# Performance work log

Measured on AMD Instinct MI355X. Metric: run time of the kernel, lower is better.

## Reference

```python
import jax, jax.numpy as jnp
import numpy as np
import math

B, S, H = 2, 2048, 2048
NH, NKV, HD = 16, 4, 128


def _rope_tables(seq_len, head_dim):
    # Standard RoPE: freqs over half dim, duplicated to full head_dim.
    inv_freq = 1.0 / (10000.0 ** (np.arange(0, head_dim, 2, dtype=np.float32) / head_dim))
    t = np.arange(seq_len, dtype=np.float32)
    freqs = np.outer(t, inv_freq)  # [S, HD/2]
    emb = np.concatenate([freqs, freqs], axis=-1)  # [S, HD]
    return jnp.asarray(np.cos(emb)), jnp.asarray(np.sin(emb))


def setup_inputs() -> dict:
    key = jax.random.key(0)
    k1, k2, k3, k4 = jax.random.split(key, 4)
    cos, sin = _rope_tables(S, HD)
    return {
        "x": jax.random.normal(k1, (B, S, H), dtype=jnp.float32),
        "cos": cos,
        "sin": sin,
        "Wq": jax.random.normal(k2, (H, NH * HD), dtype=jnp.float32) * (1.0 / math.sqrt(H)),
        "Wkv": jax.random.normal(k3, (H, 2 * NKV * HD), dtype=jnp.float32) * (1.0 / math.sqrt(H)),
        "Wo": jax.random.normal(k4, (NH * HD, H), dtype=jnp.float32) * (1.0 / math.sqrt(NH * HD)),
    }


def _rotate_half(x):
    x1, x2 = jnp.split(x, 2, axis=-1)
    return jnp.concatenate([-x2, x1], axis=-1)


def _apply_rotary(x, cos, sin):
    # x: [B, S, nheads, HD]; cos/sin: [S, HD]
    c = cos[None, :, None, :]
    s = sin[None, :, None, :]
    return x * c + _rotate_half(x) * s


def reference(x, cos, sin, Wq, Wkv, Wo):
    b, s, _ = x.shape
    q = (x @ Wq).reshape(b, s, NH, HD)
    kv = x @ Wkv
    k, v = jnp.split(kv, [NKV * HD], axis=-1)
    k = k.reshape(b, s, NKV, HD)
    v = v.reshape(b, s, NKV, HD)
    q = _apply_rotary(q, cos, sin)
    k = _apply_rotary(k, cos, sin)
    # to [B, heads, S, HD]
    q = jnp.transpose(q, (0, 2, 1, 3))
    k = jnp.transpose(k, (0, 2, 1, 3))
    v = jnp.transpose(v, (0, 2, 1, 3))
    # GQA: repeat K/V heads
    rep = NH // NKV
    k = jnp.repeat(k, rep, axis=1)
    v = jnp.repeat(v, rep, axis=1)
    scale = jnp.asarray(1.0 / math.sqrt(HD), dtype=x.dtype)
    scores = jnp.einsum('bhqd,bhkd->bhqk', q * scale, k)  # [B, NH, S, S]
    causal = jnp.tril(jnp.ones((s, s), dtype=jnp.bool_))
    scores = jnp.where(causal, scores, jnp.asarray(-jnp.inf, scores.dtype))
    attn = jax.nn.softmax(scores, axis=-1)
    out = jnp.einsum('bhqk,bhkd->bhqd', attn, v)
    out = jnp.transpose(out, (0, 2, 1, 3)).reshape(b, s, NH * HD)
    return out @ Wo
```

## Files before the change

### kernel.cpp

```cpp
#include <hip/hip_runtime.h>
#include <math.h>

#define NB 2
#define SEQ 2048
#define HDIM 2048
#define NHD 16
#define NKVH 4
#define HEADD 128
#define MROWS (NB*SEQ)
#define NQCOLS (NHD*HEADD)
#define QKVCOLS 3072

typedef unsigned short ushortT;
typedef __attribute__((ext_vector_type(8))) short short8;
typedef __attribute__((ext_vector_type(4))) float floatx4;
typedef __attribute__((ext_vector_type(4))) unsigned short ushort4v;

__device__ __forceinline__ ushortT f2bf(float f) {
  union { float f; unsigned int u; } v; v.f = f;
  unsigned int r = v.u + 0x7FFFu + ((v.u >> 16) & 1u);
  return (ushortT)(r >> 16);
}
__device__ __forceinline__ float bf2f(ushortT u) {
  union { unsigned int u; float f; } v; v.u = ((unsigned int)u) << 16;
  return v.f;
}

__device__ __forceinline__ unsigned int cvt_pk_bf16(float lo, float hi) {
  unsigned int r;
  asm("v_cvt_pk_bf16_f32 %0, %1, %2" : "=v"(r) : "v"(lo), "v"(hi));
  return r;
}

__device__ __forceinline__ void gload16(const ushortT* g, ushortT* l) {
  __builtin_amdgcn_global_load_lds(
      (const __attribute__((address_space(1))) void*)g,
      (__attribute__((address_space(3))) void*)l, 16, 0, 0);
}

__device__ __forceinline__ void tile_barrier() {
  asm volatile("" ::: "memory");
  __builtin_amdgcn_s_barrier();
  asm volatile("" ::: "memory");
  __builtin_amdgcn_sched_barrier(0);
}

__global__ __launch_bounds__(256) void cast_bf16_kernel(
    const float* __restrict__ in, ushortT* __restrict__ out, int n4) {
  int i = blockIdx.x * 256 + threadIdx.x;
  if (i >= n4) return;
  float4 v = ((const float4*)in)[i];
  ushort4v o;
  o.x = f2bf(v.x); o.y = f2bf(v.y); o.z = f2bf(v.z); o.w = f2bf(v.w);
  ((ushort4v*)out)[i] = o;
}

__global__ __launch_bounds__(256) void transpose_cast3_kernel(
    const float* __restrict__ Wq, const float* __restrict__ Wkv,
    const float* __restrict__ Wo, ushortT* __restrict__ out) {
  __shared__ ushortT tile[32][33];
  int cu0 = blockIdx.x * 32, r0 = blockIdx.y * 32;
  const float* src; int C, c0;
  if (cu0 < 2048)      { src = Wq;  C = 2048; c0 = cu0; }
  else if (cu0 < 3072) { src = Wkv; C = 1024; c0 = cu0 - 2048; }
  else                 { src = Wo;  C = 2048; c0 = cu0 - 3072; }
  int tx = threadIdx.x & 31, ty = threadIdx.x >> 5;
#pragma unroll
  for (int i = 0; i < 4; ++i)
    tile[ty + i*8][tx] = f2bf(src[(size_t)(r0 + ty + i*8) * C + c0 + tx]);
  __syncthreads();
#pragma unroll
  for (int i = 0; i < 4; ++i)
    out[(size_t)(cu0 + ty + i*8) * 2048 + r0 + tx] = tile[tx][ty + i*8];
}

template <int MH>
__global__ __launch_bounds__(512, 2) void gemm_ring_kernel(
    const ushortT* __restrict__ A, const ushortT* __restrict__ Bt,
    void* __restrict__ C, int M, int N, int K, int c_fp32) {
  constexpr int BM = 128 * MH;
  constexpr int LPT = MH + 2;
  __shared__ __align__(16) ushortT lA[4][BM * 32];
  __shared__ __align__(16) ushortT lB[4][256 * 32];
  const int m0 = blockIdx.y * BM;
  const int n0 = blockIdx.x * 256;
  const int tid = threadIdx.x;
  const int lane = tid & 63, wave = tid >> 6;
  const int g = lane >> 4, l15 = lane & 15;
  const int wr = wave >> 2, wc = wave & 3;
  const int wm = wr * (BM / 2), wn = wc * 64;

  floatx4 acc[4 * MH][4] = {};

  auto stageA = [&](int u) {
    ushortT* dst = lA[u & 3];
    const int kt = u << 5;
#pragma unroll
    for (int i = 0; i < MH; ++i) {
      int s = i * 512 + tid;
      int r = s >> 2, j = s & 3;
      int jj = j ^ ((r >> 1) & 3);
      gload16(A + (size_t)(m0 + r) * K + kt + jj * 8, dst + s * 8);
    }
  };
  auto stageB = [&](int u) {
    ushortT* dst = lB[u & 3];
    const int kt = u << 5;
#pragma unroll
    for (int i = 0; i < 2; ++i) {
      int s = i * 512 + tid;
      int r = s >> 2, j = s & 3;
      int jj = j ^ ((r >> 1) & 3);
      gload16(Bt + (size_t)(n0 + r) * K + kt + jj * 8, dst + s * 8);
    }
  };

  stageA(0); stageB(0); stageA(1); stageB(1); stageA(2); stageB(2);

  const int NT = K >> 5;
  for (int u = 0; u < NT; ++u) {
    if constexpr (MH == 2) {
      if (u + 2 < NT)      asm volatile("s_waitcnt vmcnt(8)" ::: "memory");
      else if (u + 1 < NT) asm volatile("s_waitcnt vmcnt(4)" ::: "memory");
      else                 asm volatile("s_waitcnt vmcnt(0)" ::: "memory");
    } else {
      if (u + 2 < NT)      asm volatile("s_waitcnt vmcnt(6)" ::: "memory");
      else if (u + 1 < NT) asm volatile("s_waitcnt vmcnt(3)" ::: "memory");
      else                 asm volatile("s_waitcnt vmcnt(0)" ::: "memory");
    }
    tile_barrier();

    const ushortT* la = lA[u & 3];
    const ushortT* lb = lB[u & 3];
    const bool more = (u + 3) < NT;

    short8 bfr[4];
#pragma unroll
    for (int nt = 0; nt < 4; ++nt) {
      int col = wn + nt * 16 + l15;
      bfr[nt] = *(const short8*)(lb + col * 32 + (g ^ ((col >> 1) & 3)) * 8);
    }

#pragma unroll
    for (int mh = 0; mh < MH; ++mh) {
      if (mh) tile_barrier();
      short8 afr[4];
#pragma unroll
      for (int mt = 0; mt < 4; ++mt) {
        int row = wm + mh * 64 + mt * 16 + l15;
        afr[mt] = *(const short8*)(la + row * 32 + (g ^ ((row >> 1) & 3)) * 8);
      }
      if (more) {
        if (mh == 0) stageA(u + 3);
        if (mh == MH - 1) stageB(u + 3);
      }
      __builtin_amdgcn_s_setprio(1);
#pragma unroll
      for (int mt = 0; mt < 4; ++mt)
#pragma unroll
        for (int nt = 0; nt < 4; ++nt)
          acc[mh * 4 + mt][nt] = __builtin_amdgcn_mfma_f32_16x16x32_bf16(
              afr[mt], bfr[nt], acc[mh * 4 + mt][nt], 0, 0, 0);
      __builtin_amdgcn_s_setprio(0);
    }
  }

#pragma unroll
  for (int fm = 0; fm < 4 * MH; ++fm)
#pragma unroll
    for (int nt = 0; nt < 4; ++nt)
#pragma unroll
      for (int r4 = 0; r4 < 4; ++r4) {
        int row = m0 + wm + fm * 16 + g * 4 + r4;
        int col = n0 + wn + nt * 16 + l15;
        float v = acc[fm][nt][r4];
        if (c_fp32) ((float*)C)[(size_t)row * N + col] = v;
        else ((ushortT*)C)[(size_t)row * N + col] = f2bf(v);
      }
}

__global__ __launch_bounds__(256) void rope_qk_kernel(
    const ushortT* __restrict__ QKVtmp, const float* __restrict__ cosT,
    const float* __restrict__ sinT, ushortT* __restrict__ Qr,
    ushortT* __restrict__ Kr) {
  int idx = blockIdx.x * 256 + threadIdx.x;
  if (idx < NB * SEQ * NHD * 64) {
    int d = idx & 63;
    int t = idx >> 6;
    int h = t & (NHD - 1);
    int bs = t >> 4;
    int s = bs & (SEQ - 1);
    int b = bs >> 11;
    float c = cosT[s * HEADD + d], sn = sinT[s * HEADD + d];
    float q1 = bf2f(QKVtmp[(size_t)bs * QKVCOLS + h * HEADD + d]);
    float q2 = bf2f(QKVtmp[(size_t)bs * QKVCOLS + h * HEADD + d + 64]);
    size_t o = ((size_t)(b * NHD + h) * SEQ + s) * HEADD + d;
    Qr[o]      = f2bf(q1 * c - q2 * sn);
    Qr[o + 64] = f2bf(q2 * c + q1 * sn);
  } else {
    int k = idx - NB * SEQ * NHD * 64;
    int d = k & 63;
    int t = k >> 6;
    int kvh = t & (NKVH - 1);
    int bs = t >> 2;
    int s = bs & (SEQ - 1);
    int b = bs >> 11;
    float c = cosT[s * HEADD + d], sn = sinT[s * HEADD + d];
    float k1 = bf2f(QKVtmp[(size_t)bs * QKVCOLS + 2048 + kvh * HEADD + d]);
    float k2 = bf2f(QKVtmp[(size_t)bs * QKVCOLS + 2048 + kvh * HEADD + d + 64]);
    size_t o = ((size_t)(b * NKVH + kvh) * SEQ + s) * HEADD + d;
    Kr[o]      = f2bf(k1 * c - k2 * sn);
    Kr[o + 64] = f2bf(k2 * c + k1 * sn);
  }
}

__global__ __launch_bounds__(256) void v_relayout_kernel(
    const ushortT* __restrict__ QKVtmp, ushortT* __restrict__ Vt) {
  __shared__ ushortT tile[32][33];
  int bk = blockIdx.z;
  int b = bk >> 2, kvh = bk & 3;
  int s0 = blockIdx.x * 32, d0 = blockIdx.y * 32;
  int tx = threadIdx.x & 31, ty = threadIdx.x >> 5;
#pragma unroll
  for (int i = 0; i < 4; ++i) {
    int s = s0 + ty + i * 8;
    tile[ty + i * 8][tx] =
        QKVtmp[(size_t)(b * SEQ + s) * QKVCOLS + 2560 + kvh * HEADD + d0 + tx];
  }
  __syncthreads();
#pragma unroll
  for (int i = 0; i < 4; ++i) {
    int d = d0 + ty + i * 8;
    Vt[((size_t)bk * HEADD + d) * SEQ + s0 + tx] = tile[tx][ty + i * 8];
  }
}

__global__ __launch_bounds__(256) void attn_kernel(
    const ushortT* __restrict__ Q,
    const ushortT* __restrict__ Kg,
    const ushortT* __restrict__ Vg,
    ushortT* __restrict__ Oa) {
  __shared__ __align__(16) ushortT lK[2][64 * 128];
  __shared__ __align__(16) ushortT lV[2][128 * 64];
  __shared__ __align__(16) ushortT lP[4 * 16 * 64];

  const int tid = threadIdx.x;
  const int w = tid >> 6, lane = tid & 63;
  const int g = lane >> 4, l15 = lane & 15;
  const int sw = l15 & 7;
  const int bh = blockIdx.x;
  const int b = bh >> 4, h = bh & 15;
  const int kvh = h >> 2;
  const int yi = blockIdx.y;
  const int qiA = 31 - yi;
  const int qiB = yi;
  const int nA = qiA + 1, nB = qiB + 1;

  const float SC = 0.08838834764831845f * 1.4426950408889634f;
  const float THR = 8.0f / SC;

  const ushortT* kbase = Kg + ((size_t)(b * NKVH + kvh)) * SEQ * HEADD;
  const ushortT* vbase = Vg + ((size_t)(b * NKVH + kvh)) * HEADD * SEQ;
  ushortT* pw = lP + w * 16 * 64;

  const int qwA = (qiA << 6) + w * 16;
  const int qwB = (qiB << 6) + w * 16;

  short8 qfA[4], qfB[4];
  {
    const ushortT* qpA = Q + (((size_t)(b * NHD + h)) * SEQ + qwA + l15) * HEADD + g * 8;
    const ushortT* qpB = Q + (((size_t)(b * NHD + h)) * SEQ + qwB + l15) * HEADD + g * 8;
#pragma unroll
    for (int ks = 0; ks < 4; ++ks) {
      qfA[ks] = *(const short8*)(qpA + ks * 32);
      qfB[ks] = *(const short8*)(qpB + ks * 32);
    }
  }

  floatx4 o[8] = {};
  float m_s = -INFINITY;
  float l_s = 0.f;

  auto stage = [&](int kt, int buf) {
#pragma unroll
    for (int ii = 0; ii < 4; ++ii) {
      int s = ii * 256 + tid;
      int r = s >> 4, j = (s & 15) ^ (r & 7);
      gload16(kbase + (size_t)(kt * 64 + r) * HEADD + j * 8, lK[buf] + s * 8);
    }
#pragma unroll
    for (int ii = 0; ii < 4; ++ii) {
      int s = ii * 256 + tid;
      int r = s >> 3, j = (s & 7) ^ (r & 7);
      gload16(vbase + (size_t)r * SEQ + kt * 64 + j * 8, lV[buf] + s * 8);
    }
  };

  auto compute = [&](const short8 (&qf)[4], int qw, int kt, int cur) {
    const int rel = qw - kt * 64;

    floatx4 sc4[4] = {};
    __builtin_amdgcn_s_setprio(1);
#pragma unroll
    for (int nt = 0; nt < 4; ++nt) {
      if (nt * 16 > rel + 15) continue;
#pragma unroll
      for (int ks = 0; ks < 4; ++ks) {
        short8 kf = *(const short8*)(lK[cur] + (nt * 16 + l15) * 128 + ((ks * 4 + g) ^ sw) * 8);
        sc4[nt] = __builtin_amdgcn_mfma_f32_16x16x32_bf16(kf, qf[ks], sc4[nt], 0, 0, 0);
      }
    }
    __builtin_amdgcn_s_setprio(0);

    const bool needmask = (kt * 64 + 63) > qw;
    float ps[4][4];
    float mx = -INFINITY;
#pragma unroll
    for (int nt = 0; nt < 4; ++nt)
#pragma unroll
      for (int r = 0; r < 4; ++r) {
        float v = sc4[nt][r];
        if (needmask) {
          int kg = kt * 64 + nt * 16 + g * 4 + r;
          if (kg > qw + l15) v = -INFINITY;
        }
        ps[nt][r] = v;
        mx = fmaxf(mx, v);
      }
    mx = fmaxf(mx, __shfl_xor(mx, 16));
    mx = fmaxf(mx, __shfl_xor(mx, 32));

    float mn;
    if (__all(mx <= m_s + THR)) {
      mn = m_s;
    } else {
      mn = fmaxf(m_s, mx);
      float alpha = __builtin_amdgcn_exp2f((m_s - mn) * SC);
      l_s *= alpha;
#pragma unroll
      for (int dt = 0; dt < 8; ++dt)
#pragma unroll
        for (int r = 0; r < 4; ++r) o[dt][r] *= alpha;
      m_s = mn;
    }
    const float mnSC = mn * SC;

    float rs = 0.f;
#pragma unroll
    for (int nt = 0; nt < 4; ++nt) {
      float e[4];
#pragma unroll
      for (int r = 0; r < 4; ++r) {
        e[r] = __builtin_amdgcn_exp2f(__builtin_fmaf(ps[nt][r], SC, -mnSC));
        rs += e[r];
      }
      uint2 pk;
      pk.x = cvt_pk_bf16(e[0], e[1]);
      pk.y = cvt_pk_bf16(e[2], e[3]);
      *(uint2*)(pw + l15 * 64 + (((nt * 2 + (g >> 1)) ^ sw) * 8 + (g & 1) * 4)) = pk;
    }
    rs += __shfl_xor(rs, 16);
    rs += __shfl_xor(rs, 32);
    l_s += rs;

    __builtin_amdgcn_s_setprio(1);
#pragma unroll
    for (int ks = 0; ks < 2; ++ks) {
      if (kt * 64 + ks * 32 > qw + 15) continue;
      short8 bp = *(const short8*)(pw + l15 * 64 + ((ks * 4 + g) ^ sw) * 8);
#pragma unroll
      for (int dt = 0; dt < 8; ++dt) {
        short8 vf = *(const short8*)(lV[cur] + (dt * 16 + l15) * 64 + ((ks * 4 + g) ^ sw) * 8);
        o[dt] = __builtin_amdgcn_mfma_f32_16x16x32_bf16(vf, bp, o[dt], 0, 0, 0);
      }
    }
    __builtin_amdgcn_s_setprio(0);
  };

  auto epilogue = [&](int qw) {
    float inv = 1.f / l_s;
    int qg = qw + l15;
#pragma unroll
    for (int dt = 0; dt < 8; ++dt) {
      uint2 ov;
      ov.x = cvt_pk_bf16(o[dt][0] * inv, o[dt][1] * inv);
      ov.y = cvt_pk_bf16(o[dt][2] * inv, o[dt][3] * inv);
      *(uint2*)(Oa + (size_t)(b * SEQ + qg) * NQCOLS + h * HEADD + dt * 16 + g * 4) = ov;
    }
  };

  stage(0, 0);
  asm volatile("s_waitcnt vmcnt(0)" ::: "memory");
  __builtin_amdgcn_s_barrier();

  for (int kt = 0; kt < nA; ++kt) {
    const int cur = kt & 1;
    if (kt + 1 < nA) stage(kt + 1, cur ^ 1);
    else             stage(0, cur ^ 1);
    compute(qfA, qwA, kt, cur);
    asm volatile("s_waitcnt vmcnt(0)" ::: "memory");
    __builtin_amdgcn_s_barrier();
  }
  epilogue(qwA);
#pragma unroll
  for (int dt = 0; dt < 8; ++dt) o[dt] = floatx4{0.f, 0.f, 0.f, 0.f};
  m_s = -INFINITY; l_s = 0.f;

  for (int kt = 0; kt < nB; ++kt) {
    const int cur = (nA + kt) & 1;
    if (kt + 1 < nB) stage(kt + 1, cur ^ 1);
    compute(qfB, qwB, kt, cur);
    asm volatile("s_waitcnt vmcnt(0)" ::: "memory");
    __builtin_amdgcn_s_barrier();
  }
  epilogue(qwB);
}

extern "C" void kernel_launch(void* const* d_in, const int* in_sizes, int n_in,
                              void* d_out, int out_size, void* d_ws, size_t ws_size,
                              hipStream_t stream) {
  const float* x    = (const float*)d_in[0];
  const float* cosT = (const float*)d_in[1];
  const float* sinT = (const float*)d_in[2];
  const float* Wq   = (const float*)d_in[3];
  const float* Wkv  = (const float*)d_in[4];
  const float* Wo   = (const float*)d_in[5];

  char* ws = (char*)d_ws;
  ushortT* x_bf   = (ushortT*)(ws + 0);
  ushortT* Wqkvt  = (ushortT*)(ws + 16777216);
  ushortT* Wot    = (ushortT*)(ws + 29360128);
  ushortT* QKVtmp = (ushortT*)(ws + 37748736);
  ushortT* Qr     = (ushortT*)(ws + 62914560);
  ushortT* Kr     = (ushortT*)(ws + 79691776);
  ushortT* Vt     = (ushortT*)(ws + 83886080);
  ushortT* Oattn  = QKVtmp;

  cast_bf16_kernel<<<8192, 256, 0, stream>>>(x, x_bf, (MROWS * HDIM) / 4);
  transpose_cast3_kernel<<<dim3(160, 64), 256, 0, stream>>>(Wq, Wkv, Wo, Wqkvt);

  gemm_ring_kernel<2><<<dim3(12, 16), 512, 0, stream>>>(x_bf, Wqkvt, QKVtmp,
                                                        MROWS, QKVCOLS, HDIM, 0);

  rope_qk_kernel<<<20480, 256, 0, stream>>>(QKVtmp, cosT, sinT, Qr, Kr);
  v_relayout_kernel<<<dim3(64, 4, 8), 256, 0, stream>>>(QKVtmp, Vt);

  attn_kernel<<<dim3(32, 16), 256, 0, stream>>>(Qr, Kr, Vt, Oattn);

  gemm_ring_kernel<1><<<dim3(8, 32), 512, 0, stream>>>(Oattn, Wot, d_out,
                                                       MROWS, HDIM, NQCOLS, 1);
}
```

Measured before the change: 313.6 us.

## Enlarge attention query tile to 128 rows with two m-tiles per wave

Each attention block now handles one 128-row query tile, with every wave owning 32 rows as two 16-row MFMA m-tiles. Each K and V fragment read from LDS feeds two MFMAs, cutting LDS traffic and staging per query, and loads are amortised over more work. This replaces the earlier pairing of a short and a long causal tile per block, so block work is now uneven; heavy tiles are ordered first to soften the tail. Register pressure roughly doubles for accumulators, and launch bounds now request two blocks per CU.

```diff
diff --git a/kernel.cpp b/kernel.cpp
--- a/kernel.cpp
+++ b/kernel.cpp
@@ -79,7 +79,6 @@
     const ushortT* __restrict__ A, const ushortT* __restrict__ Bt,
     void* __restrict__ C, int M, int N, int K, int c_fp32) {
   constexpr int BM = 128 * MH;
-  constexpr int LPT = MH + 2;
   __shared__ __align__(16) ushortT lA[4][BM * 32];
   __shared__ __align__(16) ushortT lB[4][256 * 32];
   const int m0 = blockIdx.y * BM;
@@ -235,14 +234,14 @@
   }
 }
 
-__global__ __launch_bounds__(256) void attn_kernel(
+__global__ __launch_bounds__(256, 2) void attn_kernel(
     const ushortT* __restrict__ Q,
     const ushortT* __restrict__ Kg,
     const ushortT* __restrict__ Vg,
     ushortT* __restrict__ Oa) {
   __shared__ __align__(16) ushortT lK[2][64 * 128];
   __shared__ __align__(16) ushortT lV[2][128 * 64];
-  __shared__ __align__(16) ushortT lP[4 * 16 * 64];
+  __shared__ __align__(16) ushortT lP[4 * 32 * 64];
 
   const int tid = threadIdx.x;
   const int w = tid >> 6, lane = tid & 63;
@@ -252,34 +251,30 @@
   const int b = bh >> 4, h = bh & 15;
   const int kvh = h >> 2;
   const int yi = blockIdx.y;
-  const int qiA = 31 - yi;
-  const int qiB = yi;
-  const int nA = qiA + 1, nB = qiB + 1;
+  const int qi = (yi < 8) ? (15 - yi) : (yi - 8);
+  const int q0 = qi << 7;
+  const int qw = q0 + w * 32;
+  const int nkt = 2 * qi + 2;
 
   const float SC = 0.08838834764831845f * 1.4426950408889634f;
   const float THR = 8.0f / SC;
 
   const ushortT* kbase = Kg + ((size_t)(b * NKVH + kvh)) * SEQ * HEADD;
   const ushortT* vbase = Vg + ((size_t)(b * NKVH + kvh)) * HEADD * SEQ;
-  ushortT* pw = lP + w * 16 * 64;
-
-  const int qwA = (qiA << 6) + w * 16;
-  const int qwB = (qiB << 6) + w * 16;
-
-  short8 qfA[4], qfB[4];
-  {
-    const ushortT* qpA = Q + (((size_t)(b * NHD + h)) * SEQ + qwA + l15) * HEADD + g * 8;
-    const ushortT* qpB = Q + (((size_t)(b * NHD + h)) * SEQ + qwB + l15) * HEADD + g * 8;
-#pragma unroll
-    for (int ks = 0; ks < 4; ++ks) {
-      qfA[ks] = *(const short8*)(qpA + ks * 32);
-      qfB[ks] = *(const short8*)(qpB + ks * 32);
-    }
-  }
-
-  floatx4 o[8] = {};
-  float m_s = -INFINITY;
-  float l_s = 0.f;
+  ushortT* pw = lP + w * 32 * 64;
+
+  short8 qf[2][4];
+#pragma unroll
+  for (int mt = 0; mt < 2; ++mt) {
+    const ushortT* qp =
+        Q + (((size_t)(b * NHD + h)) * SEQ + qw + mt * 16 + l15) * HEADD + g * 8;
+#pragma unroll
+    for (int ks = 0; ks < 4; ++ks) qf[mt][ks] = *(const short8*)(qp + ks * 32);
+  }
+
+  floatx4 o[2][8] = {};
+  float m_s[2] = {-INFINITY, -INFINITY};
+  float l_s[2] = {0.f, 0.f};
 
   auto stage = [&](int kt, int buf) {
 #pragma unroll
@@ -296,124 +291,126 @@
     }
   };
 
-  auto compute = [&](const short8 (&qf)[4], int qw, int kt, int cur) {
-    const int rel = qw - kt * 64;
-
-    floatx4 sc4[4] = {};
-    __builtin_amdgcn_s_setprio(1);
-#pragma unroll
-    for (int nt = 0; nt < 4; ++nt) {
-      if (nt * 16 > rel + 15) continue;
-#pragma unroll
-      for (int ks = 0; ks < 4; ++ks) {
-        short8 kf = *(const short8*)(lK[cur] + (nt * 16 + l15) * 128 + ((ks * 4 + g) ^ sw) * 8);
-        sc4[nt] = __builtin_amdgcn_mfma_f32_16x16x32_bf16(kf, qf[ks], sc4[nt], 0, 0, 0);
-      }
-    }
-    __builtin_amdgcn_s_setprio(0);
-
-    const bool needmask = (kt * 64 + 63) > qw;
-    float ps[4][4];
-    float mx = -INFINITY;
-#pragma unroll
-    for (int nt = 0; nt < 4; ++nt)
-#pragma unroll
-      for (int r = 0; r < 4; ++r) {
-        float v = sc4[nt][r];
-        if (needmask) {
-          int kg = kt * 64 + nt * 16 + g * 4 + r;
-          if (kg > qw + l15) v = -INFINITY;
-        }
-        ps[nt][r] = v;
-        mx = fmaxf(mx, v);
-      }
-    mx = fmaxf(mx, __shfl_xor(mx, 16));
-    mx = fmaxf(mx, __shfl_xor(mx, 32));
-
-    float mn;
-    if (__all(mx <= m_s + THR)) {
-      mn = m_s;
-    } else {
-      mn = fmaxf(m_s, mx);
-      float alpha = __builtin_amdgcn_exp2f((m_s - mn) * SC);
-      l_s *= alpha;
-#pragma unroll
-      for (int dt = 0; dt < 8; ++dt)
-#pragma unroll
-        for (int r = 0; r < 4; ++r) o[dt][r] *= alpha;
-      m_s = mn;
-    }
-    const float mnSC = mn * SC;
-
-    float rs = 0.f;
-#pragma unroll
-    for (int nt = 0; nt < 4; ++nt) {
-      float e[4];
-#pragma unroll
-      for (int r = 0; r < 4; ++r) {
-        e[r] = __builtin_amdgcn_exp2f(__builtin_fmaf(ps[nt][r], SC, -mnSC));
-        rs += e[r];
-      }
-      uint2 pk;
-      pk.x = cvt_pk_bf16(e[0], e[1]);
-      pk.y = cvt_pk_bf16(e[2], e[3]);
-      *(uint2*)(pw + l15 * 64 + (((nt * 2 + (g >> 1)) ^ sw) * 8 + (g & 1) * 4)) = pk;
-    }
-    rs += __shfl_xor(rs, 16);
-    rs += __shfl_xor(rs, 32);
-    l_s += rs;
-
-    __builtin_amdgcn_s_setprio(1);
-#pragma unroll
-    for (int ks = 0; ks < 2; ++ks) {
-      if (kt * 64 + ks * 32 > qw + 15) continue;
-      short8 bp = *(const short8*)(pw + l15 * 64 + ((ks * 4 + g) ^ sw) * 8);
-#pragma unroll
-      for (int dt = 0; dt < 8; ++dt) {
-        short8 vf = *(const short8*)(lV[cur] + (dt * 16 + l15) * 64 + ((ks * 4 + g) ^ sw) * 8);
-        o[dt] = __builtin_amdgcn_mfma_f32_16x16x32_bf16(vf, bp, o[dt], 0, 0, 0);
-      }
-    }
-    __builtin_amdgcn_s_setprio(0);
-  };
-
-  auto epilogue = [&](int qw) {
-    float inv = 1.f / l_s;
-    int qg = qw + l15;
-#pragma unroll
-    for (int dt = 0; dt < 8; ++dt) {
-      uint2 ov;
-      ov.x = cvt_pk_bf16(o[dt][0] * inv, o[dt][1] * inv);
-      ov.y = cvt_pk_bf16(o[dt][2] * inv, o[dt][3] * inv);
-      *(uint2*)(Oa + (size_t)(b * SEQ + qg) * NQCOLS + h * HEADD + dt * 16 + g * 4) = ov;
-    }
-  };
-
   stage(0, 0);
   asm volatile("s_waitcnt vmcnt(0)" ::: "memory");
   __builtin_amdgcn_s_barrier();
 
-  for (int kt = 0; kt < nA; ++kt) {
+  for (int kt = 0; kt < nkt; ++kt) {
     const int cur = kt & 1;
-    if (kt + 1 < nA) stage(kt + 1, cur ^ 1);
-    else             stage(0, cur ^ 1);
-    compute(qfA, qwA, kt, cur);
+    if (kt + 1 < nkt) stage(kt + 1, cur ^ 1);
+
+    const int kb = kt * 64;
+    const int rel0 = qw - kb;
+    const int rel1 = qw + 16 - kb;
+
+    floatx4 sc[2][4] = {};
+    __builtin_amdgcn_s_setprio(1);
+#pragma unroll
+    for (int nt = 0; nt < 4; ++nt) {
+      if (nt * 16 > rel1 + 15) continue;
+      const bool need0 = (nt * 16 <= rel0 + 15);
+#pragma unroll
+      for (int ks = 0; ks < 4; ++ks) {
+        short8 kf = *(const short8*)(lK[cur] + (nt * 16 + l15) * 128 + ((ks * 4 + g) ^ sw) * 8);
+        sc[1][nt] = __builtin_amdgcn_mfma_f32_16x16x32_bf16(kf, qf[1][ks], sc[1][nt], 0, 0, 0);
+        if (need0)
+          sc[0][nt] = __builtin_amdgcn_mfma_f32_16x16x32_bf16(kf, qf[0][ks], sc[0][nt], 0, 0, 0);
+      }
+    }
+    __builtin_amdgcn_s_setprio(0);
+
+#pragma unroll
+    for (int mt = 0; mt < 2; ++mt) {
+      const int qsub = qw + mt * 16;
+      if (kb > qsub + 15) continue;
+      const bool needmask = (kb + 63) > qsub;
+      float ps[4][4];
+      float mx = -INFINITY;
+#pragma unroll
+      for (int nt = 0; nt < 4; ++nt)
+#pragma unroll
+        for (int r = 0; r < 4; ++r) {
+          float v = sc[mt][nt][r];
+          if (needmask) {
+            int kg = kb + nt * 16 + g * 4 + r;
+            if (kg > qsub + l15) v = -INFINITY;
+          }
+          ps[nt][r] = v;
+          mx = fmaxf(mx, v);
+        }
+      mx = fmaxf(mx, __shfl_xor(mx, 16));
+      mx = fmaxf(mx, __shfl_xor(mx, 32));
+
+      float mn;
+      if (__all(mx <= m_s[mt] + THR)) {
+        mn = m_s[mt];
+      } else {
+        mn = fmaxf(m_s[mt], mx);
+        float alpha = __builtin_amdgcn_exp2f((m_s[mt] - mn) * SC);
+        l_s[mt] *= alpha;
+#pragma unroll
+        for (int dt = 0; dt < 8; ++dt)
+#pragma unroll
+          for (int r = 0; r < 4; ++r) o[mt][dt][r] *= alpha;
+        m_s[mt] = mn;
+      }
+      const float mnSC = mn * SC;
+
+      float rs = 0.f;
+#pragma unroll
+      for (int nt = 0; nt < 4; ++nt) {
+        float e[4];
+#pragma unroll
+        for (int r = 0; r < 4; ++r) {
+          e[r] = __builtin_amdgcn_exp2f(__builtin_fmaf(ps[nt][r], SC, -mnSC));
+          rs += e[r];
+        }
+        uint2 pk;
+        pk.x = cvt_pk_bf16(e[0], e[1]);
+        pk.y = cvt_pk_bf16(e[2], e[3]);
+        *(uint2*)(pw + (mt * 16 + l15) * 64 +
+                  (((nt * 2 + (g >> 1)) ^ sw) * 8 + (g & 1) * 4)) = pk;
+      }
+      rs += __shfl_xor(rs, 16);
+      rs += __shfl_xor(rs, 32);
+      l_s[mt] += rs;
+    }
+
+    __builtin_amdgcn_s_setprio(1);
+#pragma unroll
+    for (int ks = 0; ks < 2; ++ks) {
+      const bool n1 = (kb + ks * 32 <= qw + 31);
+      if (!n1) continue;
+      const bool n0 = (kb + ks * 32 <= qw + 15);
+      short8 bp1 = *(const short8*)(pw + (16 + l15) * 64 + ((ks * 4 + g) ^ sw) * 8);
+      short8 bp0;
+      if (n0) bp0 = *(const short8*)(pw + l15 * 64 + ((ks * 4 + g) ^ sw) * 8);
+#pragma unroll
+      for (int dt = 0; dt < 8; ++dt) {
+        short8 vf = *(const short8*)(lV[cur] + (dt * 16 + l15) * 64 + ((ks * 4 + g) ^ sw) * 8);
+        o[1][dt] = __builtin_amdgcn_mfma_f32_16x16x32_bf16(vf, bp1, o[1][dt], 0, 0, 0);
+        if (n0)
+          o[0][dt] = __builtin_amdgcn_mfma_f32_16x16x32_bf16(vf, bp0, o[0][dt], 0, 0, 0);
+      }
+    }
+    __builtin_amdgcn_s_setprio(0);
+
     asm volatile("s_waitcnt vmcnt(0)" ::: "memory");
     __builtin_amdgcn_s_barrier();
   }
-  epilogue(qwA);
-#pragma unroll
-  for (int dt = 0; dt < 8; ++dt) o[dt] = floatx4{0.f, 0.f, 0.f, 0.f};
-  m_s = -INFINITY; l_s = 0.f;
-
-  for (int kt = 0; kt < nB; ++kt) {
-    const int cur = (nA + kt) & 1;
-    if (kt + 1 < nB) stage(kt + 1, cur ^ 1);
-    compute(qfB, qwB, kt, cur);
-    asm volatile("s_waitcnt vmcnt(0)" ::: "memory");
-    __builtin_amdgcn_s_barrier();
-  }
-  epilogue(qwB);
+
+#pragma unroll
+  for (int mt = 0; mt < 2; ++mt) {
+    float inv = 1.f / l_s[mt];
+    int qg = qw + mt * 16 + l15;
+#pragma unroll
+    for (int dt = 0; dt < 8; ++dt) {
+      uint2 ov;
+      ov.x = cvt_pk_bf16(o[mt][dt][0] * inv, o[mt][dt][1] * inv);
+      ov.y = cvt_pk_bf16(o[mt][dt][2] * inv, o[mt][dt][3] * inv);
+      *(uint2*)(Oa + (size_t)(b * SEQ + qg) * NQCOLS + h * HEADD + dt * 16 + g * 4) = ov;
+    }
+  }
 }
 
 extern "C" void kernel_launch(void* const* d_in, const int* in_sizes, int n_in,
```

Result: slower. 344.0 us (+9.7%).
